# Performance work log

Measured on AMD Instinct MI355X. Metric: run time of the kernel, lower is better.

The kernel has to match this reference:

```python
import jax, jax.numpy as jnp
import numpy as np

EPS = 1e-6
N_LEVELS = 8
BASE_RES = 16
DESIRED_RES = 128
N_POINTS = 524288


def _grid_meta():
    # replicate DAGrid.__init__ level resolutions and flat-table offsets
    b = (DESIRED_RES / BASE_RES) ** (1.0 / (N_LEVELS - 1))
    scales, offsets = [], [0]
    for i in range(N_LEVELS):
        res = int(BASE_RES * b ** i)
        scales.append(res)
        offsets.append(offsets[-1] + (res + 1) ** 3)
    return scales, offsets


def setup_inputs() -> dict:
    key = jax.random.key(0)
    scales, offsets = _grid_meta()
    lo = np.array([-1.0, -1.0, -1.0], np.float32)
    hi_eps = np.array([1.0, 1.0, 1.0], np.float32) - EPS  # bounds[1] -= eps before anchor init
    anchors = []
    for res in scales:
        axes = [np.linspace(lo[d], hi_eps[d], res + 1, dtype=np.float32) for d in range(3)]
        g = np.stack(np.meshgrid(*axes, indexing='ij'), axis=-1).reshape(-1, 3)
        anchors.append(g)
    data = jnp.asarray(np.concatenate(anchors, axis=0))  # (T, 3) learned grid param
    xyz = jax.random.normal(key, (N_POINTS, 3), dtype=jnp.float32)
    return {
        'xyz': xyz,
        'data': data,
        'scales': jnp.asarray(scales, jnp.float32),              # (L,)
        'level_offsets': jnp.asarray(offsets[:-1], jnp.int32),   # (L,)
        'bounds': jnp.asarray(np.stack([lo, np.array([1.0, 1.0, 1.0], np.float32)])),  # (2,3) raw bbox
    }


def reference(xyz, data, scales, level_offsets, bounds):
    L = scales.shape[0]
    lo = bounds[0]
    hi = bounds[1] - EPS
    size = jnp.max(bounds[1] - bounds[0])
    x = jnp.clip(xyz, lo, hi)
    xn = (x - lo) / size                                   # (N,3) in [0,1)
    fx = xn[None, :, :] * scales[:, None, None]            # (L,N,3)
    base = jnp.floor(fx).astype(jnp.int32)                 # (L,N,3) lower corner
    off = fx - base.astype(fx.dtype)                       # (L,N,3) trilinear frac
    corners = jnp.asarray([[0, 0, 0], [0, 0, 1], [0, 1, 0], [0, 1, 1],
                           [1, 0, 0], [1, 0, 1], [1, 1, 0], [1, 1, 1]], jnp.int32)  # (8,3)
    idx = base[:, :, None, :] + corners[None, None, :, :]  # (L,N,8,3)
    r1 = (scales + 1.0).astype(jnp.int32)                  # (L,) points per axis
    ind = (idx[..., 0] * (r1 * r1)[:, None, None]
           + idx[..., 1] * r1[:, None, None]
           + idx[..., 2]
           + level_offsets[:, None, None])                 # (L,N,8) flat gather index
    val = data[ind]                                        # (L,N,8,3) gathered anchors
    cf = corners.astype(fx.dtype)
    w = jnp.clip(1.0 - cf + (2.0 * cf - 1.0) * off[:, :, None, :], 0.0, 1.0)  # (L,N,8,3)
    w = w[..., 0] * w[..., 1] * w[..., 2]                  # (L,N,8) trilinear weights
    freqs = (2.0 ** jnp.arange(L, dtype=fx.dtype))[:, None, None, None]
    enc = jnp.concatenate([jnp.sin(val * freqs), jnp.cos(val * freqs)], axis=-1)  # (L,N,8,6)
    out = jnp.einsum('lnk,lnkf->nlf', w, enc)              # (N,L,6)
    out = out.reshape(xyz.shape[0], -1)                    # (N, 6*L)
    return jnp.concatenate([xyz, out], axis=-1)            # (N, 3 + 6*L)
```

## Files before the change

kernel.cpp:

```cpp
#include <hip/hip_runtime.h>

#define NLEV 8
#define PTS_PER_BLOCK 64
#define ROW_F 51

typedef unsigned int u32x4 __attribute__((ext_vector_type(4)));

__global__ __launch_bounds__(256) void phase_repack16(
    const float* __restrict__ data,
    const int*   __restrict__ level_offsets,
    uint4* __restrict__ tab, int T)
{
    __shared__ float sv[(256 + 1) * 3];
    __shared__ int   soff[NLEV];
    const int tid  = threadIdx.x;
    const int base = blockIdx.x * 256;

    if (tid < NLEV) soff[tid] = level_offsets[tid];
    for (int k = tid; k < (256 + 1) * 3; k += 256) {
        const int gi = base * 3 + k;
        sv[k] = (gi < T * 3) ? data[gi] : 0.0f;
    }
    __syncthreads();

    const int i = base + tid;
    if (i >= T) return;

    int l = 0;
    #pragma unroll
    for (int j = 1; j < NLEV; ++j) l += (i >= soff[j]) ? 1 : 0;
    const float s = (float)(1 << l) * 0.15915494309189535f;

    unsigned q[6];
    #pragma unroll
    for (int k = 0; k < 6; ++k) {
        float f = sv[tid * 3 + k] * s;
        f -= floorf(f);
        q[k] = ((unsigned)(f * 65536.0f + 0.5f)) & 0xffffu;
    }
    tab[i] = make_uint4(q[0] | (q[1] << 16), q[2], q[3] | (q[4] << 16), q[5]);
}

__device__ __forceinline__ void sincos_rev(float r, float& sn, float& cs) {
    asm("v_sin_f32 %0, %1" : "=v"(sn) : "v"(r));
    asm("v_cos_f32 %0, %1" : "=v"(cs) : "v"(r));
}

__global__ __launch_bounds__(256, 4) void dagrid_kernel(
    const float* __restrict__ xyz,
    const uint4* __restrict__ tab,
    const float* __restrict__ scales,
    const int*   __restrict__ level_offsets,
    const float* __restrict__ bounds,
    float* __restrict__ out,
    int npts)
{
    __shared__ alignas(16) float sxyz[PTS_PER_BLOCK * 3];
    __shared__ alignas(16) float sres[PTS_PER_BLOCK][ROW_F];

    const int tid = threadIdx.x;
    const int l   = tid & 7;
    const int p   = tid >> 3;
    const int block_base = blockIdx.x * PTS_PER_BLOCK;
    const bool full_block = (block_base + PTS_PER_BLOCK <= npts);

    if (full_block) {
        if (tid < 48)
            ((float4*)sxyz)[tid] = ((const float4*)(xyz + (size_t)block_base * 3))[tid];
    } else if (tid < PTS_PER_BLOCK * 3) {
        const int gi = block_base * 3 + tid;
        sxyz[tid] = (gi < npts * 3) ? xyz[gi] : 0.0f;
    }

    const float scale = scales[l];
    const int   off_l = level_offsets[l];

    const float lox = bounds[0], loy = bounds[1], loz = bounds[2];
    const float hix = bounds[3] - 1e-6f;
    const float hiy = bounds[4] - 1e-6f;
    const float hiz = bounds[5] - 1e-6f;
    const float size = fmaxf(fmaxf(bounds[3] - bounds[0], bounds[4] - bounds[1]),
                             bounds[5] - bounds[2]);
    const float inv_size = 1.0f / size;

    __syncthreads();

    const int nA = block_base + p;
    const int nB = nA + 32;
    const bool actA = (nA < npts);
    const bool actB = (nB < npts);

    const float rxA = sxyz[p * 3 + 0], ryA = sxyz[p * 3 + 1], rzA = sxyz[p * 3 + 2];
    const float rxB = sxyz[(p + 32) * 3 + 0], ryB = sxyz[(p + 32) * 3 + 1],
                rzB = sxyz[(p + 32) * 3 + 2];

    const int r1   = (int)scale + 1;
    const int r1sq = r1 * r1;

    #define ADDR(rx, ry, rz, act, ox, oy, oz, idx)                                \
    {                                                                             \
        const float x = fminf(fmaxf(rx, lox), hix);                               \
        const float y = fminf(fmaxf(ry, loy), hiy);                               \
        const float z = fminf(fmaxf(rz, loz), hiz);                               \
        const float fx = (x - lox) * inv_size * scale;                            \
        const float fy = (y - loy) * inv_size * scale;                            \
        const float fz = (z - loz) * inv_size * scale;                            \
        const float bxf = floorf(fx), byf = floorf(fy), bzf = floorf(fz);         \
        ox = fx - bxf; oy = fy - byf; oz = fz - bzf;                              \
        idx = act ? ((int)bxf * r1sq + (int)byf * r1 + (int)bzf + off_l) : 0;     \
    }
    float oxA, oyA, ozA, oxB, oyB, ozB;
    int idxA, idxB;
    ADDR(rxA, ryA, rzA, actA, oxA, oyA, ozA, idxA)
    ADDR(rxB, ryB, rzB, actB, oxB, oyB, ozB, idxB)
    #undef ADDR

    const unsigned long long baseAddr = (unsigned long long)tab;
    const unsigned long long aA = baseAddr + 16ull * (unsigned)idxA;
    const unsigned long long aB = baseAddr + 16ull * (unsigned)idxB;
    const unsigned long long sY = 16ull * (unsigned)r1;
    const unsigned long long sX = 16ull * (unsigned)r1sq;

    u32x4 eA0, eA1, eA2, eA3, eB0, eB1, eB2, eB3;
    #define GLOAD(dst, addr) \
        asm volatile("global_load_dwordx4 %0, %1, off" : "=&v"(dst) : "v"(addr))
    GLOAD(eA0, aA);
    GLOAD(eA1, aA + sY);
    GLOAD(eA2, aA + sX);
    GLOAD(eA3, aA + sX + sY);
    GLOAD(eB0, aB);
    GLOAD(eB1, aB + sY);
    GLOAD(eB2, aB + sX);
    GLOAD(eB3, aB + sX + sY);
    #undef GLOAD
    asm volatile("s_waitcnt vmcnt(0)"
                 : "+v"(eA0), "+v"(eA1), "+v"(eA2), "+v"(eA3),
                   "+v"(eB0), "+v"(eB1), "+v"(eB2), "+v"(eB3));
    __builtin_amdgcn_sched_barrier(0);

    const float K = 1.0f / 65536.0f;

    #define PAIRE(e, WXY, oz_, wz0_, a0, a1, a2, a3, a4, a5)                      \
    {                                                                             \
        const float w0 = (WXY) * (wz0_);                                          \
        const float w1 = (WXY) * (oz_);                                           \
        float sn, cs;                                                             \
        sincos_rev((float)(e.x & 0xffffu) * K, sn, cs); a0 += w0*sn; a3 += w0*cs; \
        sincos_rev((float)(e.x >> 16)     * K, sn, cs); a1 += w0*sn; a4 += w0*cs; \
        sincos_rev((float)(e.y)           * K, sn, cs); a2 += w0*sn; a5 += w0*cs; \
        sincos_rev((float)(e.z & 0xffffu) * K, sn, cs); a0 += w1*sn; a3 += w1*cs; \
        sincos_rev((float)(e.z >> 16)     * K, sn, cs); a1 += w1*sn; a4 += w1*cs; \
        sincos_rev((float)(e.w)           * K, sn, cs); a2 += w1*sn; a5 += w1*cs; \
    }

    float a0 = 0.f, a1 = 0.f, a2 = 0.f, a3 = 0.f, a4 = 0.f, a5 = 0.f;
    {
        const float wz0 = 1.0f - ozA;
        const float wx0 = 1.0f - oxA, wy0 = 1.0f - oyA;
        PAIRE(eA0, wx0 * wy0, ozA, wz0, a0, a1, a2, a3, a4, a5)
        PAIRE(eA1, wx0 * oyA, ozA, wz0, a0, a1, a2, a3, a4, a5)
        PAIRE(eA2, oxA * wy0, ozA, wz0, a0, a1, a2, a3, a4, a5)
        PAIRE(eA3, oxA * oyA, ozA, wz0, a0, a1, a2, a3, a4, a5)
    }
    float b0 = 0.f, b1 = 0.f, b2 = 0.f, b3 = 0.f, b4 = 0.f, b5 = 0.f;
    {
        const float wz0 = 1.0f - ozB;
        const float wx0 = 1.0f - oxB, wy0 = 1.0f - oyB;
        PAIRE(eB0, wx0 * wy0, ozB, wz0, b0, b1, b2, b3, b4, b5)
        PAIRE(eB1, wx0 * oyB, ozB, wz0, b0, b1, b2, b3, b4, b5)
        PAIRE(eB2, oxB * wy0, ozB, wz0, b0, b1, b2, b3, b4, b5)
        PAIRE(eB3, oxB * oyB, ozB, wz0, b0, b1, b2, b3, b4, b5)
    }
    #undef PAIRE

    {
        const int c = 3 + l * 6;
        float* rowA = sres[p];
        rowA[c + 0] = a0; rowA[c + 1] = a1; rowA[c + 2] = a2;
        rowA[c + 3] = a3; rowA[c + 4] = a4; rowA[c + 5] = a5;
        float* rowB = sres[p + 32];
        rowB[c + 0] = b0; rowB[c + 1] = b1; rowB[c + 2] = b2;
        rowB[c + 3] = b3; rowB[c + 4] = b4; rowB[c + 5] = b5;
        if (l == 0) {
            rowA[0] = rxA; rowA[1] = ryA; rowA[2] = rzA;
            rowB[0] = rxB; rowB[1] = ryB; rowB[2] = rzB;
        }
    }
    __syncthreads();

    if (full_block) {
        const float4* flat4 = (const float4*)&sres[0][0];
        float4* ob4 = (float4*)(out + (size_t)block_base * ROW_F);
        for (int i = tid; i < (PTS_PER_BLOCK * ROW_F) / 4; i += 256)
            ob4[i] = flat4[i];
    } else {
        const float* flat = &sres[0][0];
        float* ob = out + (size_t)block_base * ROW_F;
        const int lim = npts * ROW_F - block_base * ROW_F;
        for (int i = tid; i < PTS_PER_BLOCK * ROW_F; i += 256)
            if (i < lim) ob[i] = flat[i];
    }
}

typedef float f4u __attribute__((ext_vector_type(4), aligned(4)));
typedef float f2u __attribute__((ext_vector_type(2), aligned(4)));

__global__ __launch_bounds__(256) void dagrid_kernel_direct(
    const float* __restrict__ xyz,
    const float* __restrict__ data,
    const float* __restrict__ scales,
    const int*   __restrict__ level_offsets,
    const float* __restrict__ bounds,
    float* __restrict__ out,
    int npts)
{
    __shared__ alignas(16) float sxyz[32 * 3];
    __shared__ alignas(16) float sres[32][ROW_F];

    const int tid = threadIdx.x;
    const int l   = tid & 7;
    const int p   = tid >> 3;
    const int block_base = blockIdx.x * 32;

    if (tid < 32 * 3) {
        const int gi = block_base * 3 + tid;
        sxyz[tid] = (gi < npts * 3) ? xyz[gi] : 0.0f;
    }
    const float scale = scales[l];
    const int   off_l = level_offsets[l];
    const float lox = bounds[0], loy = bounds[1], loz = bounds[2];
    const float hix = bounds[3] - 1e-6f;
    const float hiy = bounds[4] - 1e-6f;
    const float hiz = bounds[5] - 1e-6f;
    const float size = fmaxf(fmaxf(bounds[3] - bounds[0], bounds[4] - bounds[1]),
                             bounds[5] - bounds[2]);
    const float inv_size = 1.0f / size;
    __syncthreads();

    const int n = block_base + p;
    const bool active = (n < npts);
    const float rx = sxyz[p * 3 + 0];
    const float ry = sxyz[p * 3 + 1];
    const float rz = sxyz[p * 3 + 2];
    float acc0 = 0.f, acc1 = 0.f, acc2 = 0.f, acc3 = 0.f, acc4 = 0.f, acc5 = 0.f;

    if (active) {
        const float x = fminf(fmaxf(rx, lox), hix);
        const float y = fminf(fmaxf(ry, loy), hiy);
        const float z = fminf(fmaxf(rz, loz), hiz);
        const float xn = (x - lox) * inv_size;
        const float yn = (y - loy) * inv_size;
        const float zn = (z - loz) * inv_size;
        const int r1 = (int)scale + 1;
        const int r1sq = r1 * r1;
        const float fx = xn * scale, fy = yn * scale, fz = zn * scale;
        const float bxf = floorf(fx), byf = floorf(fy), bzf = floorf(fz);
        const float ox = fx - bxf, oy = fy - byf, oz = fz - bzf;
        const int i000 = (int)bxf * r1sq + (int)byf * r1 + (int)bzf + off_l;
        const float* p0 = data + 3 * (size_t)i000;
        const float* p1 = p0 + 3 * r1;
        const float* p2 = p0 + 3 * r1sq;
        const float* p3 = p2 + 3 * r1;
        const f4u q0 = *(const f4u*)p0;  const f2u g0 = *(const f2u*)(p0 + 4);
        const f4u q1 = *(const f4u*)p1;  const f2u g1 = *(const f2u*)(p1 + 4);
        const f4u q2 = *(const f4u*)p2;  const f2u g2 = *(const f2u*)(p2 + 4);
        const f4u q3 = *(const f4u*)p3;  const f2u g3 = *(const f2u*)(p3 + 4);
        const float freq = (float)(1 << l);
        const float wz0 = 1.0f - oz;
        const float wx1 = ox, wx0 = 1.0f - ox;
        const float wy1 = oy, wy0 = 1.0f - oy;
        float sn, cs;
        #define PAIR(a, b, WXY)                                                   \
        {                                                                         \
            const float w0 = (WXY) * wz0;                                         \
            const float w1 = (WXY) * oz;                                          \
            __sincosf(a.x * freq, &sn, &cs); acc0 += w0 * sn; acc3 += w0 * cs;    \
            __sincosf(a.y * freq, &sn, &cs); acc1 += w0 * sn; acc4 += w0 * cs;    \
            __sincosf(a.z * freq, &sn, &cs); acc2 += w0 * sn; acc5 += w0 * cs;    \
            __sincosf(a.w * freq, &sn, &cs); acc0 += w1 * sn; acc3 += w1 * cs;    \
            __sincosf(b.x * freq, &sn, &cs); acc1 += w1 * sn; acc4 += w1 * cs;    \
            __sincosf(b.y * freq, &sn, &cs); acc2 += w1 * sn; acc5 += w1 * cs;    \
        }
        PAIR(q0, g0, wx0 * wy0)
        PAIR(q1, g1, wx0 * wy1)
        PAIR(q2, g2, wx1 * wy0)
        PAIR(q3, g3, wx1 * wy1)
        #undef PAIR
    }
    {
        float* row = sres[p];
        const int c = 3 + l * 6;
        row[c + 0] = acc0; row[c + 1] = acc1; row[c + 2] = acc2;
        row[c + 3] = acc3; row[c + 4] = acc4; row[c + 5] = acc5;
        if (l == 0) { row[0] = rx; row[1] = ry; row[2] = rz; }
    }
    __syncthreads();
    {
        const float* flat = &sres[0][0];
        float* ob = out + (size_t)block_base * ROW_F;
        const int lim = npts * ROW_F - block_base * ROW_F;
        for (int i = tid; i < 32 * ROW_F; i += 256)
            if (i < lim) ob[i] = flat[i];
    }
}

extern "C" void kernel_launch(void* const* d_in, const int* in_sizes, int n_in,
                              void* d_out, int out_size, void* d_ws, size_t ws_size,
                              hipStream_t stream) {
    const float* xyz           = (const float*)d_in[0];
    const float* data          = (const float*)d_in[1];
    const float* scales        = (const float*)d_in[2];
    const int*   level_offsets = (const int*)d_in[3];
    const float* bounds        = (const float*)d_in[4];
    float* out = (float*)d_out;

    const int npts = in_sizes[0] / 3;
    const int T    = in_sizes[1] / 3;

    const size_t ws_needed = (size_t)T * sizeof(uint4);
    if (d_ws != nullptr && ws_size >= ws_needed) {
        uint4* tab = (uint4*)d_ws;
        phase_repack16<<<(T + 255) / 256, 256, 0, stream>>>(data, level_offsets, tab, T);
        const int nblocks = (npts + PTS_PER_BLOCK - 1) / PTS_PER_BLOCK;
        dagrid_kernel<<<nblocks, 256, 0, stream>>>(xyz, tab, scales, level_offsets,
                                                   bounds, out, npts);
    } else {
        const int nblocks = (npts + 31) / 32;
        dagrid_kernel_direct<<<nblocks, 256, 0, stream>>>(xyz, data, scales,
                                                          level_offsets, bounds,
                                                          out, npts);
    }
}
```

Baseline: 153.6 us.

## Spatially sort points by Morton bin before grid gather for cache locality

Adds a counting-sort pipeline (histogram, single-block scan, scatter) that groups points into 32^3 Morton-ordered bins, so the main kernel processes spatially nearby points together and its grid-table gathers hit cache more often. Results are scattered back to the original point order row by row. Workgroup IDs are remapped so that contiguous sorted chunks land on the same XCD. The cost is four extra launches, atomics, a serial scan and uncoalesced output writes. The fallback path is replaced by an 8-byte table variant, and the direct-data path is removed.

Result: slower. 324.6 us (+111.3%).

```diff
diff --git a/kernel.cpp b/kernel.cpp
--- a/kernel.cpp
+++ b/kernel.cpp
@@ -3,18 +3,21 @@
 #define NLEV 8
 #define PTS_PER_BLOCK 64
 #define ROW_F 51
+#define NBIN 32768
 
 typedef unsigned int u32x4 __attribute__((ext_vector_type(4)));
 
 __global__ __launch_bounds__(256) void phase_repack16(
     const float* __restrict__ data,
     const int*   __restrict__ level_offsets,
-    uint4* __restrict__ tab, int T)
+    uint4* __restrict__ tab, unsigned* __restrict__ hist, int T)
 {
     __shared__ float sv[(256 + 1) * 3];
     __shared__ int   soff[NLEV];
     const int tid  = threadIdx.x;
     const int base = blockIdx.x * 256;
+
+    if (blockIdx.x < NBIN / 256) hist[blockIdx.x * 256 + tid] = 0u;
 
     if (tid < NLEV) soff[tid] = level_offsets[tid];
     for (int k = tid; k < (256 + 1) * 3; k += 256) {
@@ -41,54 +44,151 @@
     tab[i] = make_uint4(q[0] | (q[1] << 16), q[2], q[3] | (q[4] << 16), q[5]);
 }
 
+__device__ __forceinline__ unsigned mexp5(unsigned v) {
+    v = (v | (v << 8)) & 0x100Fu;
+    v = (v | (v << 4)) & 0x10C3u;
+    v = (v | (v << 2)) & 0x1249u;
+    return v;
+}
+__device__ __forceinline__ unsigned point_bin(
+    float x, float y, float z,
+    float lox, float loy, float loz,
+    float hix, float hiy, float hiz, float inv_size)
+{
+    const float xn = (fminf(fmaxf(x, lox), hix) - lox) * inv_size;
+    const float yn = (fminf(fmaxf(y, loy), hiy) - loy) * inv_size;
+    const float zn = (fminf(fmaxf(z, loz), hiz) - loz) * inv_size;
+    const int bx = min(31, (int)(xn * 32.0f));
+    const int by = min(31, (int)(yn * 32.0f));
+    const int bz = min(31, (int)(zn * 32.0f));
+    return mexp5((unsigned)bx) | (mexp5((unsigned)by) << 1) | (mexp5((unsigned)bz) << 2);
+}
+
+#define LOAD_BOUNDS                                                              \
+    const float lox = bounds[0], loy = bounds[1], loz = bounds[2];               \
+    const float hix = bounds[3] - 1e-6f;                                         \
+    const float hiy = bounds[4] - 1e-6f;                                         \
+    const float hiz = bounds[5] - 1e-6f;                                         \
+    const float size = fmaxf(fmaxf(bounds[3] - bounds[0], bounds[4] - bounds[1]),\
+                             bounds[5] - bounds[2]);                             \
+    const float inv_size = 1.0f / size;
+
+__global__ __launch_bounds__(256) void sort_hist(
+    const float* __restrict__ xyz, const float* __restrict__ bounds,
+    unsigned* __restrict__ hist, int npts)
+{
+    __shared__ float sv[256 * 3];
+    const int tid = threadIdx.x;
+    const int base = blockIdx.x * 256;
+    for (int k = tid; k < 256 * 3; k += 256) {
+        const int gi = base * 3 + k;
+        sv[k] = (gi < npts * 3) ? xyz[gi] : 0.0f;
+    }
+    LOAD_BOUNDS
+    __syncthreads();
+    const int i = base + tid;
+    if (i >= npts) return;
+    const unsigned b = point_bin(sv[tid*3], sv[tid*3+1], sv[tid*3+2],
+                                 lox, loy, loz, hix, hiy, hiz, inv_size);
+    atomicAdd(&hist[b], 1u);
+}
+
+__global__ __launch_bounds__(256) void sort_scan(
+    const unsigned* __restrict__ hist, unsigned* __restrict__ offs)
+{
+    __shared__ unsigned sdat[256];
+    const int tid = threadIdx.x;
+    unsigned carry = 0;
+    for (int c = 0; c < NBIN / 256; ++c) {
+        const int i = c * 256 + tid;
+        const unsigned v = hist[i];
+        sdat[tid] = v;
+        __syncthreads();
+        #pragma unroll
+        for (int off = 1; off < 256; off <<= 1) {
+            const unsigned t = (tid >= off) ? sdat[tid - off] : 0u;
+            __syncthreads();
+            sdat[tid] += t;
+            __syncthreads();
+        }
+        offs[i] = carry + sdat[tid] - v;
+        const unsigned tot = sdat[255];
+        __syncthreads();
+        carry += tot;
+    }
+}
+
+__global__ __launch_bounds__(256) void sort_scatter(
+    const float* __restrict__ xyz, const float* __restrict__ bounds,
+    unsigned* __restrict__ offs, int* __restrict__ g_sidx,
+    float* __restrict__ g_sxyz, int npts)
+{
+    __shared__ float sv[256 * 3];
+    const int tid = threadIdx.x;
+    const int base = blockIdx.x * 256;
+    for (int k = tid; k < 256 * 3; k += 256) {
+        const int gi = base * 3 + k;
+        sv[k] = (gi < npts * 3) ? xyz[gi] : 0.0f;
+    }
+    LOAD_BOUNDS
+    __syncthreads();
+    const int i = base + tid;
+    if (i >= npts) return;
+    const float x = sv[tid*3], y = sv[tid*3+1], z = sv[tid*3+2];
+    const unsigned b = point_bin(x, y, z, lox, loy, loz, hix, hiy, hiz, inv_size);
+    const unsigned pos = atomicAdd(&offs[b], 1u);
+    g_sidx[pos] = i;
+    g_sxyz[pos * 3 + 0] = x;
+    g_sxyz[pos * 3 + 1] = y;
+    g_sxyz[pos * 3 + 2] = z;
+}
+
 __device__ __forceinline__ void sincos_rev(float r, float& sn, float& cs) {
     asm("v_sin_f32 %0, %1" : "=v"(sn) : "v"(r));
     asm("v_cos_f32 %0, %1" : "=v"(cs) : "v"(r));
 }
 
-__global__ __launch_bounds__(256, 4) void dagrid_kernel(
-    const float* __restrict__ xyz,
+__global__ __launch_bounds__(256, 4) void dagrid_sorted(
+    const float* __restrict__ g_sxyz,
+    const int*   __restrict__ g_sidx,
     const uint4* __restrict__ tab,
     const float* __restrict__ scales,
     const int*   __restrict__ level_offsets,
     const float* __restrict__ bounds,
     float* __restrict__ out,
-    int npts)
+    int npts, int nwg)
 {
     __shared__ alignas(16) float sxyz[PTS_PER_BLOCK * 3];
     __shared__ alignas(16) float sres[PTS_PER_BLOCK][ROW_F];
+    __shared__ int sidx_l[PTS_PER_BLOCK];
+
+    const int orig = blockIdx.x;
+    const int qq = nwg >> 3, rr = nwg & 7;
+    const int xcd = orig & 7, ii = orig >> 3;
+    const int bid = (xcd < rr ? xcd * (qq + 1) : rr * (qq + 1) + (xcd - rr) * qq) + ii;
 
     const int tid = threadIdx.x;
     const int l   = tid & 7;
     const int p   = tid >> 3;
-    const int block_base = blockIdx.x * PTS_PER_BLOCK;
+    const int block_base = bid * PTS_PER_BLOCK;
     const bool full_block = (block_base + PTS_PER_BLOCK <= npts);
 
     if (full_block) {
         if (tid < 48)
-            ((float4*)sxyz)[tid] = ((const float4*)(xyz + (size_t)block_base * 3))[tid];
+            ((float4*)sxyz)[tid] = ((const float4*)(g_sxyz + (size_t)block_base * 3))[tid];
     } else if (tid < PTS_PER_BLOCK * 3) {
         const int gi = block_base * 3 + tid;
-        sxyz[tid] = (gi < npts * 3) ? xyz[gi] : 0.0f;
+        sxyz[tid] = (gi < npts * 3) ? g_sxyz[gi] : 0.0f;
+    }
+    if (tid < PTS_PER_BLOCK) {
+        const int pos = block_base + tid;
+        sidx_l[tid] = (pos < npts) ? g_sidx[pos] : -1;
     }
 
     const float scale = scales[l];
     const int   off_l = level_offsets[l];
-
-    const float lox = bounds[0], loy = bounds[1], loz = bounds[2];
-    const float hix = bounds[3] - 1e-6f;
-    const float hiy = bounds[4] - 1e-6f;
-    const float hiz = bounds[5] - 1e-6f;
-    const float size = fmaxf(fmaxf(bounds[3] - bounds[0], bounds[4] - bounds[1]),
-                             bounds[5] - bounds[2]);
-    const float inv_size = 1.0f / size;
-
-    __syncthreads();
-
-    const int nA = block_base + p;
-    const int nB = nA + 32;
-    const bool actA = (nA < npts);
-    const bool actB = (nB < npts);
+    LOAD_BOUNDS
+    __syncthreads();
 
     const float rxA = sxyz[p * 3 + 0], ryA = sxyz[p * 3 + 1], rzA = sxyz[p * 3 + 2];
     const float rxB = sxyz[(p + 32) * 3 + 0], ryB = sxyz[(p + 32) * 3 + 1],
@@ -96,6 +196,8 @@
 
     const int r1   = (int)scale + 1;
     const int r1sq = r1 * r1;
+    const bool actA = (block_base + p) < npts;
+    const bool actB = (block_base + p + 32) < npts;
 
     #define ADDR(rx, ry, rz, act, ox, oy, oz, idx)                                \
     {                                                                             \
@@ -188,6 +290,167 @@
     }
     __syncthreads();
 
+    {
+        const int r = tid >> 2;
+        const int j = tid & 3;
+        const int orig_i = sidx_l[r];
+        if (orig_i >= 0) {
+            float* ob = out + (size_t)orig_i * ROW_F;
+            #pragma unroll
+            for (int k = 0; k < 13; ++k) {
+                const int ci = j + 4 * k;
+                if (ci < ROW_F) ob[ci] = sres[r][ci];
+            }
+        }
+    }
+}
+
+typedef unsigned int u4a8 __attribute__((ext_vector_type(4), aligned(8)));
+
+__global__ __launch_bounds__(256) void phase_repack8(
+    const float* __restrict__ data,
+    const int*   __restrict__ level_offsets,
+    uint2* __restrict__ tab, int T)
+{
+    __shared__ float sv[256 * 3];
+    __shared__ int   soff[NLEV];
+    const int tid  = threadIdx.x;
+    const int base = blockIdx.x * 256;
+    if (tid < NLEV) soff[tid] = level_offsets[tid];
+    for (int k = tid; k < 256 * 3; k += 256) {
+        const int gi = base * 3 + k;
+        sv[k] = (gi < T * 3) ? data[gi] : 0.0f;
+    }
+    __syncthreads();
+    const int i = base + tid;
+    if (i >= T) return;
+    int l = 0;
+    #pragma unroll
+    for (int j = 1; j < NLEV; ++j) l += (i >= soff[j]) ? 1 : 0;
+    const float s = (float)(1 << l) * 0.15915494309189535f;
+    unsigned q[3];
+    #pragma unroll
+    for (int k = 0; k < 3; ++k) {
+        float f = sv[tid * 3 + k] * s;
+        f -= floorf(f);
+        q[k] = ((unsigned)(f * 65536.0f + 0.5f)) & 0xffffu;
+    }
+    tab[i] = make_uint2(q[0] | (q[1] << 16), q[2]);
+}
+
+__global__ __launch_bounds__(256, 4) void dagrid_kernel8(
+    const float* __restrict__ xyz,
+    const uint2* __restrict__ tab,
+    const float* __restrict__ scales,
+    const int*   __restrict__ level_offsets,
+    const float* __restrict__ bounds,
+    float* __restrict__ out,
+    int npts)
+{
+    __shared__ alignas(16) float sxyz[PTS_PER_BLOCK * 3];
+    __shared__ alignas(16) float sres[PTS_PER_BLOCK][ROW_F];
+
+    const int tid = threadIdx.x;
+    const int l   = tid & 7;
+    const int p   = tid >> 3;
+    const int block_base = blockIdx.x * PTS_PER_BLOCK;
+    const bool full_block = (block_base + PTS_PER_BLOCK <= npts);
+
+    if (full_block) {
+        if (tid < 48)
+            ((float4*)sxyz)[tid] = ((const float4*)(xyz + (size_t)block_base * 3))[tid];
+    } else if (tid < PTS_PER_BLOCK * 3) {
+        const int gi = block_base * 3 + tid;
+        sxyz[tid] = (gi < npts * 3) ? xyz[gi] : 0.0f;
+    }
+    const float scale = scales[l];
+    const int   off_l = level_offsets[l];
+    LOAD_BOUNDS
+    __syncthreads();
+
+    const float rxA = sxyz[p * 3 + 0], ryA = sxyz[p * 3 + 1], rzA = sxyz[p * 3 + 2];
+    const float rxB = sxyz[(p + 32) * 3 + 0], ryB = sxyz[(p + 32) * 3 + 1],
+                rzB = sxyz[(p + 32) * 3 + 2];
+    const int r1   = (int)scale + 1;
+    const int r1sq = r1 * r1;
+    const bool actA = (block_base + p) < npts;
+    const bool actB = (block_base + p + 32) < npts;
+
+    #define ADDR(rx, ry, rz, act, ox, oy, oz, idx)                                \
+    {                                                                             \
+        const float x = fminf(fmaxf(rx, lox), hix);                               \
+        const float y = fminf(fmaxf(ry, loy), hiy);                               \
+        const float z = fminf(fmaxf(rz, loz), hiz);                               \
+        const float fx = (x - lox) * inv_size * scale;                            \
+        const float fy = (y - loy) * inv_size * scale;                            \
+        const float fz = (z - loz) * inv_size * scale;                            \
+        const float bxf = floorf(fx), byf = floorf(fy), bzf = floorf(fz);         \
+        ox = fx - bxf; oy = fy - byf; oz = fz - bzf;                              \
+        idx = act ? ((int)bxf * r1sq + (int)byf * r1 + (int)bzf + off_l) : 0;     \
+    }
+    float oxA, oyA, ozA, oxB, oyB, ozB;
+    int idxA, idxB;
+    ADDR(rxA, ryA, rzA, actA, oxA, oyA, ozA, idxA)
+    ADDR(rxB, ryB, rzB, actB, oxB, oyB, ozB, idxB)
+    #undef ADDR
+
+    const u4a8 eA0 = *(const u4a8*)(tab + idxA);
+    const u4a8 eA1 = *(const u4a8*)(tab + idxA + r1);
+    const u4a8 eA2 = *(const u4a8*)(tab + idxA + r1sq);
+    const u4a8 eA3 = *(const u4a8*)(tab + idxA + r1sq + r1);
+    const u4a8 eB0 = *(const u4a8*)(tab + idxB);
+    const u4a8 eB1 = *(const u4a8*)(tab + idxB + r1);
+    const u4a8 eB2 = *(const u4a8*)(tab + idxB + r1sq);
+    const u4a8 eB3 = *(const u4a8*)(tab + idxB + r1sq + r1);
+
+    const float K = 1.0f / 65536.0f;
+    #define PAIRE(e, WXY, oz_, wz0_, a0, a1, a2, a3, a4, a5)                      \
+    {                                                                             \
+        const float w0 = (WXY) * (wz0_);                                          \
+        const float w1 = (WXY) * (oz_);                                           \
+        float sn, cs;                                                             \
+        sincos_rev((float)(e.x & 0xffffu) * K, sn, cs); a0 += w0*sn; a3 += w0*cs; \
+        sincos_rev((float)(e.x >> 16)     * K, sn, cs); a1 += w0*sn; a4 += w0*cs; \
+        sincos_rev((float)(e.y)           * K, sn, cs); a2 += w0*sn; a5 += w0*cs; \
+        sincos_rev((float)(e.z & 0xffffu) * K, sn, cs); a0 += w1*sn; a3 += w1*cs; \
+        sincos_rev((float)(e.z >> 16)     * K, sn, cs); a1 += w1*sn; a4 += w1*cs; \
+        sincos_rev((float)(e.w)           * K, sn, cs); a2 += w1*sn; a5 += w1*cs; \
+    }
+    float a0 = 0.f, a1 = 0.f, a2 = 0.f, a3 = 0.f, a4 = 0.f, a5 = 0.f;
+    {
+        const float wz0 = 1.0f - ozA;
+        const float wx0 = 1.0f - oxA, wy0 = 1.0f - oyA;
+        PAIRE(eA0, wx0 * wy0, ozA, wz0, a0, a1, a2, a3, a4, a5)
+        PAIRE(eA1, wx0 * oyA, ozA, wz0, a0, a1, a2, a3, a4, a5)
+        PAIRE(eA2, oxA * wy0, ozA, wz0, a0, a1, a2, a3, a4, a5)
+        PAIRE(eA3, oxA * oyA, ozA, wz0, a0, a1, a2, a3, a4, a5)
+    }
+    float b0 = 0.f, b1 = 0.f, b2 = 0.f, b3 = 0.f, b4 = 0.f, b5 = 0.f;
+    {
+        const float wz0 = 1.0f - ozB;
+        const float wx0 = 1.0f - oxB, wy0 = 1.0f - oyB;
+        PAIRE(eB0, wx0 * wy0, ozB, wz0, b0, b1, b2, b3, b4, b5)
+        PAIRE(eB1, wx0 * oyB, ozB, wz0, b0, b1, b2, b3, b4, b5)
+        PAIRE(eB2, oxB * wy0, ozB, wz0, b0, b1, b2, b3, b4, b5)
+        PAIRE(eB3, oxB * oyB, ozB, wz0, b0, b1, b2, b3, b4, b5)
+    }
+    #undef PAIRE
+
+    {
+        const int c = 3 + l * 6;
+        float* rowA = sres[p];
+        rowA[c + 0] = a0; rowA[c + 1] = a1; rowA[c + 2] = a2;
+        rowA[c + 3] = a3; rowA[c + 4] = a4; rowA[c + 5] = a5;
+        float* rowB = sres[p + 32];
+        rowB[c + 0] = b0; rowB[c + 1] = b1; rowB[c + 2] = b2;
+        rowB[c + 3] = b3; rowB[c + 4] = b4; rowB[c + 5] = b5;
+        if (l == 0) {
+            rowA[0] = rxA; rowA[1] = ryA; rowA[2] = rzA;
+            rowB[0] = rxB; rowB[1] = ryB; rowB[2] = rzB;
+        }
+    }
+    __syncthreads();
+
     if (full_block) {
         const float4* flat4 = (const float4*)&sres[0][0];
         float4* ob4 = (float4*)(out + (size_t)block_base * ROW_F);
@@ -202,108 +465,6 @@
     }
 }
 
-typedef float f4u __attribute__((ext_vector_type(4), aligned(4)));
-typedef float f2u __attribute__((ext_vector_type(2), aligned(4)));
-
-__global__ __launch_bounds__(256) void dagrid_kernel_direct(
-    const float* __restrict__ xyz,
-    const float* __restrict__ data,
-    const float* __restrict__ scales,
-    const int*   __restrict__ level_offsets,
-    const float* __restrict__ bounds,
-    float* __restrict__ out,
-    int npts)
-{
-    __shared__ alignas(16) float sxyz[32 * 3];
-    __shared__ alignas(16) float sres[32][ROW_F];
-
-    const int tid = threadIdx.x;
-    const int l   = tid & 7;
-    const int p   = tid >> 3;
-    const int block_base = blockIdx.x * 32;
-
-    if (tid < 32 * 3) {
-        const int gi = block_base * 3 + tid;
-        sxyz[tid] = (gi < npts * 3) ? xyz[gi] : 0.0f;
-    }
-    const float scale = scales[l];
-    const int   off_l = level_offsets[l];
-    const float lox = bounds[0], loy = bounds[1], loz = bounds[2];
-    const float hix = bounds[3] - 1e-6f;
-    const float hiy = bounds[4] - 1e-6f;
-    const float hiz = bounds[5] - 1e-6f;
-    const float size = fmaxf(fmaxf(bounds[3] - bounds[0], bounds[4] - bounds[1]),
-                             bounds[5] - bounds[2]);
-    const float inv_size = 1.0f / size;
-    __syncthreads();
-
-    const int n = block_base + p;
-    const bool active = (n < npts);
-    const float rx = sxyz[p * 3 + 0];
-    const float ry = sxyz[p * 3 + 1];
-    const float rz = sxyz[p * 3 + 2];
-    float acc0 = 0.f, acc1 = 0.f, acc2 = 0.f, acc3 = 0.f, acc4 = 0.f, acc5 = 0.f;
-
-    if (active) {
-        const float x = fminf(fmaxf(rx, lox), hix);
-        const float y = fminf(fmaxf(ry, loy), hiy);
-        const float z = fminf(fmaxf(rz, loz), hiz);
-        const float xn = (x - lox) * inv_size;
-        const float yn = (y - loy) * inv_size;
-        const float zn = (z - loz) * inv_size;
-        const int r1 = (int)scale + 1;
-        const int r1sq = r1 * r1;
-        const float fx = xn * scale, fy = yn * scale, fz = zn * scale;
-        const float bxf = floorf(fx), byf = floorf(fy), bzf = floorf(fz);
-        const float ox = fx - bxf, oy = fy - byf, oz = fz - bzf;
-        const int i000 = (int)bxf * r1sq + (int)byf * r1 + (int)bzf + off_l;
-        const float* p0 = data + 3 * (size_t)i000;
-        const float* p1 = p0 + 3 * r1;
-        const float* p2 = p0 + 3 * r1sq;
-        const float* p3 = p2 + 3 * r1;
-        const f4u q0 = *(const f4u*)p0;  const f2u g0 = *(const f2u*)(p0 + 4);
-        const f4u q1 = *(const f4u*)p1;  const f2u g1 = *(const f2u*)(p1 + 4);
-        const f4u q2 = *(const f4u*)p2;  const f2u g2 = *(const f2u*)(p2 + 4);
-        const f4u q3 = *(const f4u*)p3;  const f2u g3 = *(const f2u*)(p3 + 4);
-        const float freq = (float)(1 << l);
-        const float wz0 = 1.0f - oz;
-        const float wx1 = ox, wx0 = 1.0f - ox;
-        const float wy1 = oy, wy0 = 1.0f - oy;
-        float sn, cs;
-        #define PAIR(a, b, WXY)                                                   \
-        {                                                                         \
-            const float w0 = (WXY) * wz0;                                         \
-            const float w1 = (WXY) * oz;                                          \
-            __sincosf(a.x * freq, &sn, &cs); acc0 += w0 * sn; acc3 += w0 * cs;    \
-            __sincosf(a.y * freq, &sn, &cs); acc1 += w0 * sn; acc4 += w0 * cs;    \
-            __sincosf(a.z * freq, &sn, &cs); acc2 += w0 * sn; acc5 += w0 * cs;    \
-            __sincosf(a.w * freq, &sn, &cs); acc0 += w1 * sn; acc3 += w1 * cs;    \
-            __sincosf(b.x * freq, &sn, &cs); acc1 += w1 * sn; acc4 += w1 * cs;    \
-            __sincosf(b.y * freq, &sn, &cs); acc2 += w1 * sn; acc5 += w1 * cs;    \
-        }
-        PAIR(q0, g0, wx0 * wy0)
-        PAIR(q1, g1, wx0 * wy1)
-        PAIR(q2, g2, wx1 * wy0)
-        PAIR(q3, g3, wx1 * wy1)
-        #undef PAIR
-    }
-    {
-        float* row = sres[p];
-        const int c = 3 + l * 6;
-        row[c + 0] = acc0; row[c + 1] = acc1; row[c + 2] = acc2;
-        row[c + 3] = acc3; row[c + 4] = acc4; row[c + 5] = acc5;
-        if (l == 0) { row[0] = rx; row[1] = ry; row[2] = rz; }
-    }
-    __syncthreads();
-    {
-        const float* flat = &sres[0][0];
-        float* ob = out + (size_t)block_base * ROW_F;
-        const int lim = npts * ROW_F - block_base * ROW_F;
-        for (int i = tid; i < 32 * ROW_F; i += 256)
-            if (i < lim) ob[i] = flat[i];
-    }
-}
-
 extern "C" void kernel_launch(void* const* d_in, const int* in_sizes, int n_in,
                               void* d_out, int out_size, void* d_ws, size_t ws_size,
                               hipStream_t stream) {
@@ -316,18 +477,37 @@
 
     const int npts = in_sizes[0] / 3;
     const int T    = in_sizes[1] / 3;
-
-    const size_t ws_needed = (size_t)T * sizeof(uint4);
-    if (d_ws != nullptr && ws_size >= ws_needed) {
-        uint4* tab = (uint4*)d_ws;
-        phase_repack16<<<(T + 255) / 256, 256, 0, stream>>>(data, level_offsets, tab, T);
+    const int N    = npts;
+
+    const size_t off_tab  = 0;
+    const size_t off_hist = (size_t)T * 16;
+    const size_t off_offs = off_hist + (size_t)NBIN * 4;
+    const size_t off_sidx = off_offs + (size_t)NBIN * 4;
+    const size_t off_sxyz = off_sidx + (size_t)N * 4;
+    const size_t need_full = off_sxyz + (size_t)N * 12;
+
+    char* ws = (char*)d_ws;
+    if (d_ws != nullptr && ws_size >= need_full) {
+        uint4*    tab    = (uint4*)(ws + off_tab);
+        unsigned* hist   = (unsigned*)(ws + off_hist);
+        unsigned* offs   = (unsigned*)(ws + off_offs);
+        int*      g_sidx = (int*)(ws + off_sidx);
+        float*    g_sxyz = (float*)(ws + off_sxyz);
+
+        phase_repack16<<<(T + 255) / 256, 256, 0, stream>>>(data, level_offsets,
+                                                            tab, hist, T);
+        sort_hist<<<(N + 255) / 256, 256, 0, stream>>>(xyz, bounds, hist, N);
+        sort_scan<<<1, 256, 0, stream>>>(hist, offs);
+        sort_scatter<<<(N + 255) / 256, 256, 0, stream>>>(xyz, bounds, offs,
+                                                          g_sidx, g_sxyz, N);
+        const int nwg = (N + PTS_PER_BLOCK - 1) / PTS_PER_BLOCK;
+        dagrid_sorted<<<nwg, 256, 0, stream>>>(g_sxyz, g_sidx, tab, scales,
+                                               level_offsets, bounds, out, N, nwg);
+    } else if (d_ws != nullptr && ws_size >= (size_t)T * 8) {
+        uint2* tab = (uint2*)d_ws;
+        phase_repack8<<<(T + 255) / 256, 256, 0, stream>>>(data, level_offsets, tab, T);
         const int nblocks = (npts + PTS_PER_BLOCK - 1) / PTS_PER_BLOCK;
-        dagrid_kernel<<<nblocks, 256, 0, stream>>>(xyz, tab, scales, level_offsets,
-                                                   bounds, out, npts);
-    } else {
-        const int nblocks = (npts + 31) / 32;
-        dagrid_kernel_direct<<<nblocks, 256, 0, stream>>>(xyz, data, scales,
-                                                          level_offsets, bounds,
-                                                          out, npts);
-    }
-}
+        dagrid_kernel8<<<nblocks, 256, 0, stream>>>(xyz, tab, scales, level_offsets,
+                                                    bounds, out, npts);
+    }
+}
```
